# Kernel tuning notes

Hardware: AMD Instinct MI355X
Metric: run time of the kernel (lower is better)

Reference implementation:

```python
import jax, jax.numpy as jnp
import numpy as np

N_NODES = 100000


def gcn_conv(x, W, b, src, dst, n):
    """PyG GCNConv: add self-loops, sym-normalize, aggregate, linear, bias.
    out = D^{-1/2} (A + I) D^{-1/2} (x @ W) + b
    """
    h = x @ W  # [n, out]
    loops = jnp.arange(n, dtype=src.dtype)
    src_all = jnp.concatenate([src, loops])  # [E + n]
    dst_all = jnp.concatenate([dst, loops])
    # degree including self-loops (edge weights = 1)
    deg = jax.ops.segment_sum(jnp.ones_like(dst_all, dtype=h.dtype), dst_all,
                              num_segments=n)
    dinv = jax.lax.rsqrt(deg)  # deg >= 1 thanks to self-loops
    norm = dinv[src_all] * dinv[dst_all]  # [E + n]
    msg = h[src_all] * norm[:, None]      # gather + scale
    out = jax.ops.segment_sum(msg, dst_all, num_segments=n)  # scatter-add
    return out + b


def setup_inputs() -> dict:
    key = jax.random.key(0)
    k1, k2, k3, k4, k5, k6 = jax.random.split(key, 6)
    hidden = 128
    n, e = N_NODES, 1600000
    x = jax.random.normal(k1, (n, 2), dtype=jnp.float32)
    edge_index = jax.random.randint(k2, (2, e), 0, n, dtype=jnp.int32)
    # Glorot-ish init for linear weights, zero bias (PyG default)
    W1 = jax.random.normal(k3, (2, hidden), dtype=jnp.float32) * (1.0 / np.sqrt(2.0))
    b1 = jnp.zeros((hidden,), dtype=jnp.float32)
    W2 = jax.random.normal(k4, (hidden, 1), dtype=jnp.float32) * (1.0 / np.sqrt(hidden))
    b2 = jnp.zeros((1,), dtype=jnp.float32)
    return {"x": x, "edge_index": edge_index, "W1": W1, "b1": b1,
            "W2": W2, "b2": b2}


def reference(x, edge_index, W1, b1, W2, b2):
    # eval mode: dropout(p=0.5) is identity
    src, dst = edge_index[0], edge_index[1]
    n = x.shape[0]
    h = gcn_conv(x, W1, b1, src, dst, n)
    h = jax.nn.relu(h)
    out = gcn_conv(h, W2, b2, src, dst, n)  # [n, 1]
    return out
```

## Files before the change

kernel.cpp:

```cpp
#include <hip/hip_runtime.h>
#include <stdint.h>


#define BKT    256
#define LBITS  9
#define LMASK  511
#define MAXNB  512
#define MAXH   128
#define NQ     2
#define SSLOT  64
#define SSTR   68
#define SENTV  511u

#define FP_SCALE 4194304.0f
#define FP_INV   (1.0f / 4194304.0f)
#define FP_BIAS  (1 << 25)
#define A2_SCALE 262144.0f
#define A2_INV   (1.0f / 262144.0f)

__device__ __forceinline__ int bucket_of(int d, unsigned long long Mdiv) {
  return (int)(((unsigned long long)(unsigned)d * Mdiv) >> 42);
}

__device__ __forceinline__ unsigned long long pack_fp(const float2 v) {
  int ix = __float2int_rn(v.x * FP_SCALE);
  int iy = __float2int_rn(v.y * FP_SCALE);
  return ((unsigned long long)(unsigned int)iy << 32) | (unsigned int)(ix + FP_BIAS);
}

static __global__ __launch_bounds__(1024) void
k_scatter(const int* __restrict__ src, const int* __restrict__ dst,
          unsigned int* __restrict__ edges, unsigned int* __restrict__ cnt2,
          int E, int NBv, unsigned long long Mdiv, int chunk) {
  __shared__ unsigned int stage[BKT * SSTR];
  __shared__ int cntL[BKT];
  const int t = threadIdx.x, w = blockIdx.x;
  if (t < BKT) cntL[t] = 0;
  __syncthreads();

  const int e0 = w * chunk;
  const int e1 = min(e0 + chunk, E);
  unsigned int pk[4 * NQ];
  int bk[4 * NQ];
#pragma unroll
  for (int q = 0; q < NQ; ++q) {
    const int e = e0 + 4 * (t + q * 1024);
    if (e + 3 < e1) {
      int4 s4 = *reinterpret_cast<const int4*>(src + e);
      int4 d4 = *reinterpret_cast<const int4*>(dst + e);
      int b0 = bucket_of(d4.x, Mdiv), b1_ = bucket_of(d4.y, Mdiv);
      int b2_ = bucket_of(d4.z, Mdiv), b3 = bucket_of(d4.w, Mdiv);
      bk[4*q+0] = b0;  pk[4*q+0] = ((unsigned)s4.x << LBITS) | (unsigned)(d4.x - b0 * NBv);
      bk[4*q+1] = b1_; pk[4*q+1] = ((unsigned)s4.y << LBITS) | (unsigned)(d4.y - b1_ * NBv);
      bk[4*q+2] = b2_; pk[4*q+2] = ((unsigned)s4.z << LBITS) | (unsigned)(d4.z - b2_ * NBv);
      bk[4*q+3] = b3;  pk[4*q+3] = ((unsigned)s4.w << LBITS) | (unsigned)(d4.w - b3 * NBv);
    } else {
#pragma unroll
      for (int j = 0; j < 4; ++j) {
        const int ee = e + j;
        if (ee < e1) {
          int d = dst[ee];
          int bb = bucket_of(d, Mdiv);
          bk[4*q+j] = bb;
          pk[4*q+j] = ((unsigned)src[ee] << LBITS) | (unsigned)(d - bb * NBv);
        } else bk[4*q+j] = -1;
      }
    }
  }
#pragma unroll
  for (int j = 0; j < 4 * NQ; ++j) {
    if (bk[j] >= 0) {
      int p = atomicAdd(&cntL[bk[j]], 1);
      if (p < SSLOT) stage[bk[j] * SSTR + p] = pk[j];
    }
  }
  __syncthreads();
  if (t < BKT) {
    int c = min(cntL[t], SSLOT);
    cnt2[t * BKT + w] = (unsigned)c;
    int c4e = (c + 3) & ~3;
    for (int j = c; j < c4e; ++j) stage[t * SSTR + j] = SENTV;
    cntL[t] = c4e;
  }
  __syncthreads();
  const int i = t >> 2, sub = t & 3;
  const int c4 = cntL[i] >> 2;
  unsigned int* gdst = edges + (size_t)(i * BKT + w) * (size_t)SSLOT;
  const uint4* ls = reinterpret_cast<const uint4*>(stage + i * SSTR);
  for (int k = sub; k < c4; k += 4)
    *reinterpret_cast<uint4*>(gdst + (k << 2)) = ls[k];
}

static __global__ __launch_bounds__(1024) void
k_degscale(const float2* __restrict__ x, const unsigned int* __restrict__ edges,
           const unsigned int* __restrict__ cnt2, int* __restrict__ deg,
           float* __restrict__ dinv, float2* __restrict__ xs,
           unsigned long long* __restrict__ pxs, int n, int NBv) {
  __shared__ int cnt[MAXNB];
  const int b = blockIdx.x, t = threadIdx.x;
  if (t < MAXNB) cnt[t] = 0;
  __syncthreads();
  const int wrun = t >> 2, sub = t & 3;
  const int c4 = ((int)cnt2[b * BKT + wrun] + 3) >> 2;
  const uint4* run = reinterpret_cast<const uint4*>(
      edges + (size_t)(b * BKT + wrun) * (size_t)SSLOT);
  for (int k = sub; k < c4; k += 4) {
    uint4 v = run[k];
    atomicAdd(&cnt[v.x & LMASK], 1);
    atomicAdd(&cnt[v.y & LMASK], 1);
    atomicAdd(&cnt[v.z & LMASK], 1);
    atomicAdd(&cnt[v.w & LMASK], 1);
  }
  __syncthreads();
  const int l = t, node = b * NBv + l;
  if (l < NBv && node < n) {
    int c = cnt[l];
    deg[node] = c;
    float di = rsqrtf((float)(c + 1));
    dinv[node] = di;
    float2 xv = x[node];
    float2 o; o.x = di * xv.x; o.y = di * xv.y;
    xs[node] = o;
    pxs[node] = pack_fp(o);
  }
}

static __global__ __launch_bounds__(1024) void
k_agg1mlp(const unsigned int* __restrict__ edges, const unsigned int* __restrict__ cnt2,
          const int* __restrict__ deg, const float* __restrict__ dinv,
          const float2* __restrict__ xs, const unsigned long long* __restrict__ pxs,
          const float* __restrict__ W1, const float* __restrict__ b1,
          const float* __restrict__ W2, float* __restrict__ ss,
          int n, int NBv, int hidden) {
  __shared__ unsigned long long acc[MAXNB];
  __shared__ float sW1[2 * MAXH];
  __shared__ float sb1[MAXH];
  __shared__ float sW2[MAXH];
  const int b = blockIdx.x, t = threadIdx.x;
  if (t < MAXNB) acc[t] = 0ULL;
  if (t < 2 * hidden) sW1[t] = W1[t];
  if (t < hidden) { sb1[t] = b1[t]; sW2[t] = W2[t]; }
  __syncthreads();
  const int wrun = t >> 2, sub = t & 3;
  const int c4 = ((int)cnt2[b * BKT + wrun] + 3) >> 2;
  const uint4* run = reinterpret_cast<const uint4*>(
      edges + (size_t)(b * BKT + wrun) * (size_t)SSLOT);
  for (int k = sub; k < c4; k += 4) {
    uint4 v = run[k];
    atomicAdd(&acc[v.x & LMASK], pxs[v.x >> LBITS]);
    atomicAdd(&acc[v.y & LMASK], pxs[v.y >> LBITS]);
    atomicAdd(&acc[v.z & LMASK], pxs[v.z >> LBITS]);
    atomicAdd(&acc[v.w & LMASK], pxs[v.w >> LBITS]);
  }
  __syncthreads();
  const int l = t, node = b * NBv + l;
  if (l < NBv && node < n) {
    unsigned long long p = acc[l];
    long long lo = (long long)(p & 0xffffffffULL);
    long long cntv = (long long)deg[node];
    float ax = (float)(lo - cntv * (long long)FP_BIAS) * FP_INV;
    float ay = (float)((int)(unsigned int)(p >> 32)) * FP_INV;
    float di = dinv[node];
    float2 xv = xs[node];
    float a0 = di * (ax + xv.x);
    float a1 = di * (ay + xv.y);
    float sv = 0.0f;
#pragma unroll 8
    for (int j = 0; j < hidden; ++j) {
      float h = fmaf(a0, sW1[j], fmaf(a1, sW1[hidden + j], sb1[j]));
      h = fmaxf(h, 0.0f);
      sv = fmaf(h, sW2[j], sv);
    }
    ss[node] = di * sv;
  }
}

static __global__ __launch_bounds__(1024) void
k_agg2final(const unsigned int* __restrict__ edges, const unsigned int* __restrict__ cnt2,
            const float* __restrict__ dinv, const float* __restrict__ ss,
            const float* __restrict__ b2, float* __restrict__ out,
            int n, int NBv) {
  __shared__ int acc2[MAXNB];
  const int b = blockIdx.x, t = threadIdx.x;
  if (t < MAXNB) acc2[t] = 0;
  __syncthreads();
  const int wrun = t >> 2, sub = t & 3;
  const int c4 = ((int)cnt2[b * BKT + wrun] + 3) >> 2;
  const uint4* run = reinterpret_cast<const uint4*>(
      edges + (size_t)(b * BKT + wrun) * (size_t)SSLOT);
  for (int k = sub; k < c4; k += 4) {
    uint4 v = run[k];
    atomicAdd(&acc2[v.x & LMASK], __float2int_rn(ss[v.x >> LBITS] * A2_SCALE));
    atomicAdd(&acc2[v.y & LMASK], __float2int_rn(ss[v.y >> LBITS] * A2_SCALE));
    atomicAdd(&acc2[v.z & LMASK], __float2int_rn(ss[v.z >> LBITS] * A2_SCALE));
    atomicAdd(&acc2[v.w & LMASK], __float2int_rn(ss[v.w >> LBITS] * A2_SCALE));
  }
  __syncthreads();
  const int l = t, node = b * NBv + l;
  if (l < NBv && node < n)
    out[node] = dinv[node] * ((float)acc2[l] * A2_INV + ss[node]) + b2[0];
}

extern "C" void kernel_launch(void* const* d_in, const int* in_sizes, int n_in,
                              void* d_out, int out_size, void* d_ws, size_t ws_size,
                              hipStream_t stream) {
  const float2* x = (const float2*)d_in[0];
  const int*   ei = (const int*)d_in[1];
  const float* W1 = (const float*)d_in[2];
  const float* b1 = (const float*)d_in[3];
  const float* W2 = (const float*)d_in[4];
  const float* b2 = (const float*)d_in[5];

  int n = in_sizes[0] / 2;
  int E = in_sizes[1] / 2;
  int hidden = in_sizes[3];
  const int* src = ei;
  const int* dst = ei + E;
  float* out = (float*)d_out;

  int NBv = (n + BKT - 1) / BKT;
  unsigned long long Mdiv =
      ((1ULL << 42) + (unsigned long long)NBv - 1) / (unsigned long long)NBv;
  int chunk = ((E + BKT - 1) / BKT + 3) & ~3;

  char* ws = (char*)d_ws;
  unsigned int* cnt2 = (unsigned int*)ws;
  size_t o = 4LL * BKT * BKT;
  int*   deg  = (int*)(ws + o);
  float* dinv = (float*)(ws + o + 4LL * n);
  float* ss   = (float*)(ws + o + 8LL * n);
  float2* xs  = (float2*)(ws + o + 12LL * n);
  size_t poff = (o + 20LL * n + 7) & ~7LL;
  unsigned long long* pxs = (unsigned long long*)(ws + poff);
  size_t eoff = (poff + 8LL * n + 255) & ~255LL;
  unsigned int* edges = (unsigned int*)(ws + eoff);

  k_scatter<<<BKT, 1024, 0, stream>>>(src, dst, edges, cnt2, E, NBv, Mdiv, chunk);
  k_degscale<<<BKT, 1024, 0, stream>>>(x, edges, cnt2, deg, dinv, xs, pxs, n, NBv);
  k_agg1mlp<<<BKT, 1024, 0, stream>>>(edges, cnt2, deg, dinv, xs, pxs, W1, b1, W2, ss, n, NBv, hidden);
  k_agg2final<<<BKT, 1024, 0, stream>>>(edges, cnt2, dinv, ss, b2, out, n, NBv);
}
```

Measured before the change: 39.12 us.

## Split each bucket's aggregation across two workgroups by local node range

The three aggregation kernels now launch twice as many workgroups, with each pair sharing a bucket and each handling half of the bucket's local node range. Each workgroup still streams every edge of the bucket but only performs LDS atomics and gathers for edges whose destination falls in its half. Launch bounds gain an occupancy hint. The aim is to fill more compute units (512 workgroups instead of 256) at the cost of reading each bucket's edge list twice.

```diff
diff --git a/kernel.cpp b/kernel.cpp
--- a/kernel.cpp
+++ b/kernel.cpp
@@ -91,13 +91,16 @@
     *reinterpret_cast<uint4*>(gdst + (k << 2)) = ls[k];
 }
 
-static __global__ __launch_bounds__(1024) void
+
+static __global__ __launch_bounds__(1024, 8) void
 k_degscale(const float2* __restrict__ x, const unsigned int* __restrict__ edges,
            const unsigned int* __restrict__ cnt2, int* __restrict__ deg,
            float* __restrict__ dinv, float2* __restrict__ xs,
-           unsigned long long* __restrict__ pxs, int n, int NBv) {
+           unsigned long long* __restrict__ pxs, int n, int NBv, int HNB) {
   __shared__ int cnt[MAXNB];
-  const int b = blockIdx.x, t = threadIdx.x;
+  const int wg = blockIdx.x, t = threadIdx.x;
+  const int b = wg >> 1;
+  const unsigned lo = (wg & 1) * HNB;
   if (t < MAXNB) cnt[t] = 0;
   __syncthreads();
   const int wrun = t >> 2, sub = t & 3;
@@ -106,14 +109,15 @@
       edges + (size_t)(b * BKT + wrun) * (size_t)SSLOT);
   for (int k = sub; k < c4; k += 4) {
     uint4 v = run[k];
-    atomicAdd(&cnt[v.x & LMASK], 1);
-    atomicAdd(&cnt[v.y & LMASK], 1);
-    atomicAdd(&cnt[v.z & LMASK], 1);
-    atomicAdd(&cnt[v.w & LMASK], 1);
-  }
-  __syncthreads();
-  const int l = t, node = b * NBv + l;
-  if (l < NBv && node < n) {
+    unsigned lx = v.x & LMASK, ly = v.y & LMASK, lz = v.z & LMASK, lw = v.w & LMASK;
+    if (lx - lo < (unsigned)HNB) atomicAdd(&cnt[lx], 1);
+    if (ly - lo < (unsigned)HNB) atomicAdd(&cnt[ly], 1);
+    if (lz - lo < (unsigned)HNB) atomicAdd(&cnt[lz], 1);
+    if (lw - lo < (unsigned)HNB) atomicAdd(&cnt[lw], 1);
+  }
+  __syncthreads();
+  const int l = (int)lo + t, node = b * NBv + l;
+  if (t < HNB && l < NBv && node < n) {
     int c = cnt[l];
     deg[node] = c;
     float di = rsqrtf((float)(c + 1));
@@ -125,18 +129,20 @@
   }
 }
 
-static __global__ __launch_bounds__(1024) void
+static __global__ __launch_bounds__(1024, 8) void
 k_agg1mlp(const unsigned int* __restrict__ edges, const unsigned int* __restrict__ cnt2,
           const int* __restrict__ deg, const float* __restrict__ dinv,
           const float2* __restrict__ xs, const unsigned long long* __restrict__ pxs,
           const float* __restrict__ W1, const float* __restrict__ b1,
           const float* __restrict__ W2, float* __restrict__ ss,
-          int n, int NBv, int hidden) {
+          int n, int NBv, int HNB, int hidden) {
   __shared__ unsigned long long acc[MAXNB];
   __shared__ float sW1[2 * MAXH];
   __shared__ float sb1[MAXH];
   __shared__ float sW2[MAXH];
-  const int b = blockIdx.x, t = threadIdx.x;
+  const int wg = blockIdx.x, t = threadIdx.x;
+  const int b = wg >> 1;
+  const unsigned lo = (wg & 1) * HNB;
   if (t < MAXNB) acc[t] = 0ULL;
   if (t < 2 * hidden) sW1[t] = W1[t];
   if (t < hidden) { sb1[t] = b1[t]; sW2[t] = W2[t]; }
@@ -147,18 +153,19 @@
       edges + (size_t)(b * BKT + wrun) * (size_t)SSLOT);
   for (int k = sub; k < c4; k += 4) {
     uint4 v = run[k];
-    atomicAdd(&acc[v.x & LMASK], pxs[v.x >> LBITS]);
-    atomicAdd(&acc[v.y & LMASK], pxs[v.y >> LBITS]);
-    atomicAdd(&acc[v.z & LMASK], pxs[v.z >> LBITS]);
-    atomicAdd(&acc[v.w & LMASK], pxs[v.w >> LBITS]);
-  }
-  __syncthreads();
-  const int l = t, node = b * NBv + l;
-  if (l < NBv && node < n) {
+    unsigned lx = v.x & LMASK, ly = v.y & LMASK, lz = v.z & LMASK, lw = v.w & LMASK;
+    if (lx - lo < (unsigned)HNB) atomicAdd(&acc[lx], pxs[v.x >> LBITS]);
+    if (ly - lo < (unsigned)HNB) atomicAdd(&acc[ly], pxs[v.y >> LBITS]);
+    if (lz - lo < (unsigned)HNB) atomicAdd(&acc[lz], pxs[v.z >> LBITS]);
+    if (lw - lo < (unsigned)HNB) atomicAdd(&acc[lw], pxs[v.w >> LBITS]);
+  }
+  __syncthreads();
+  const int l = (int)lo + t, node = b * NBv + l;
+  if (t < HNB && l < NBv && node < n) {
     unsigned long long p = acc[l];
-    long long lo = (long long)(p & 0xffffffffULL);
+    long long lov = (long long)(p & 0xffffffffULL);
     long long cntv = (long long)deg[node];
-    float ax = (float)(lo - cntv * (long long)FP_BIAS) * FP_INV;
+    float ax = (float)(lov - cntv * (long long)FP_BIAS) * FP_INV;
     float ay = (float)((int)(unsigned int)(p >> 32)) * FP_INV;
     float di = dinv[node];
     float2 xv = xs[node];
@@ -175,13 +182,15 @@
   }
 }
 
-static __global__ __launch_bounds__(1024) void
+static __global__ __launch_bounds__(1024, 8) void
 k_agg2final(const unsigned int* __restrict__ edges, const unsigned int* __restrict__ cnt2,
             const float* __restrict__ dinv, const float* __restrict__ ss,
             const float* __restrict__ b2, float* __restrict__ out,
-            int n, int NBv) {
+            int n, int NBv, int HNB) {
   __shared__ int acc2[MAXNB];
-  const int b = blockIdx.x, t = threadIdx.x;
+  const int wg = blockIdx.x, t = threadIdx.x;
+  const int b = wg >> 1;
+  const unsigned lo = (wg & 1) * HNB;
   if (t < MAXNB) acc2[t] = 0;
   __syncthreads();
   const int wrun = t >> 2, sub = t & 3;
@@ -190,14 +199,15 @@
       edges + (size_t)(b * BKT + wrun) * (size_t)SSLOT);
   for (int k = sub; k < c4; k += 4) {
     uint4 v = run[k];
-    atomicAdd(&acc2[v.x & LMASK], __float2int_rn(ss[v.x >> LBITS] * A2_SCALE));
-    atomicAdd(&acc2[v.y & LMASK], __float2int_rn(ss[v.y >> LBITS] * A2_SCALE));
-    atomicAdd(&acc2[v.z & LMASK], __float2int_rn(ss[v.z >> LBITS] * A2_SCALE));
-    atomicAdd(&acc2[v.w & LMASK], __float2int_rn(ss[v.w >> LBITS] * A2_SCALE));
-  }
-  __syncthreads();
-  const int l = t, node = b * NBv + l;
-  if (l < NBv && node < n)
+    unsigned lx = v.x & LMASK, ly = v.y & LMASK, lz = v.z & LMASK, lw = v.w & LMASK;
+    if (lx - lo < (unsigned)HNB) atomicAdd(&acc2[lx], __float2int_rn(ss[v.x >> LBITS] * A2_SCALE));
+    if (ly - lo < (unsigned)HNB) atomicAdd(&acc2[ly], __float2int_rn(ss[v.y >> LBITS] * A2_SCALE));
+    if (lz - lo < (unsigned)HNB) atomicAdd(&acc2[lz], __float2int_rn(ss[v.z >> LBITS] * A2_SCALE));
+    if (lw - lo < (unsigned)HNB) atomicAdd(&acc2[lw], __float2int_rn(ss[v.w >> LBITS] * A2_SCALE));
+  }
+  __syncthreads();
+  const int l = (int)lo + t, node = b * NBv + l;
+  if (t < HNB && l < NBv && node < n)
     out[node] = dinv[node] * ((float)acc2[l] * A2_INV + ss[node]) + b2[0];
 }
 
@@ -219,6 +229,7 @@
   float* out = (float*)d_out;
 
   int NBv = (n + BKT - 1) / BKT;
+  int HNB = (NBv + 1) / 2;
   unsigned long long Mdiv =
       ((1ULL << 42) + (unsigned long long)NBv - 1) / (unsigned long long)NBv;
   int chunk = ((E + BKT - 1) / BKT + 3) & ~3;
@@ -236,7 +247,7 @@
   unsigned int* edges = (unsigned int*)(ws + eoff);
 
   k_scatter<<<BKT, 1024, 0, stream>>>(src, dst, edges, cnt2, E, NBv, Mdiv, chunk);
-  k_degscale<<<BKT, 1024, 0, stream>>>(x, edges, cnt2, deg, dinv, xs, pxs, n, NBv);
-  k_agg1mlp<<<BKT, 1024, 0, stream>>>(edges, cnt2, deg, dinv, xs, pxs, W1, b1, W2, ss, n, NBv, hidden);
-  k_agg2final<<<BKT, 1024, 0, stream>>>(edges, cnt2, dinv, ss, b2, out, n, NBv);
-}
+  k_degscale<<<2 * BKT, 1024, 0, stream>>>(x, edges, cnt2, deg, dinv, xs, pxs, n, NBv, HNB);
+  k_agg1mlp<<<2 * BKT, 1024, 0, stream>>>(edges, cnt2, deg, dinv, xs, pxs, W1, b1, W2, ss, n, NBv, HNB, hidden);
+  k_agg2final<<<2 * BKT, 1024, 0, stream>>>(edges, cnt2, dinv, ss, b2, out, n, NBv, HNB);
+}
```

Result: slower. 43.48 us (+11.2%).
